# Kernel tuning notes

Measured on AMD Instinct MI355X. Metric: run time of the kernel, lower is better.

Reference implementation:

```python
import jax, jax.numpy as jnp
import numpy as np

H = 64          # hidden_dim
TF = 24         # forecast_length


def _a_norm(N):
    # Complete graph (all i!=j) + GCNConv default self-loops => A+I = ones(N,N).
    # deg_i = N, so D^-1/2 (A+I) D^-1/2 = ones / N. Built generically below.
    A = jnp.ones((N, N), dtype=jnp.float32)
    deg = A.sum(axis=1)
    return A / jnp.sqrt(deg[:, None] * deg[None, :])


def _gcn(x, A, W, b):
    # PyG GCNConv: aggregate(norm * (x W)) + bias
    return jnp.einsum('ij,...jh->...ih', A, x @ W) + b


def setup_inputs() -> dict:
    key = jax.random.key(0)
    ks = jax.random.split(key, 20)
    B, N, T = 32, 128, 96
    s = lambda k, shape, fan: (jax.random.normal(k, shape, jnp.float32) / np.sqrt(max(fan, 1)))
    return {
        'x': jax.random.normal(ks[0], (B, N, T), jnp.float32),
        # spatial GCN stack
        'W_s1': s(ks[1], (1, H), 1), 'b_s1': jnp.zeros((H,), jnp.float32),
        'W_s2': s(ks[2], (H, H), H), 'b_s2': jnp.zeros((H,), jnp.float32),
        # temporal attention MLP
        'Wa1': s(ks[3], (H, H), H), 'ba1': jnp.zeros((H,), jnp.float32),
        'Wa2': s(ks[4], (H, 1), H), 'ba2': jnp.zeros((1,), jnp.float32),
        # GRU (single step, h0 = 0)
        'W_ih': s(ks[5], (3 * H, H), H), 'W_hh': s(ks[6], (3 * H, H), H),
        'b_ih': jnp.zeros((3 * H,), jnp.float32), 'b_hh': jnp.zeros((3 * H,), jnp.float32),
        # ODE-func GCN stack
        'W_o1': s(ks[7], (H, H), H), 'b_o1': jnp.zeros((H,), jnp.float32),
        'W_o2': s(ks[8], (H, H), H), 'b_o2': jnp.zeros((H,), jnp.float32),
        # output head
        'W_out': s(ks[9], (H, 1), H), 'b_out': jnp.zeros((1,), jnp.float32),
    }


def reference(x, W_s1, b_s1, W_s2, b_s2, Wa1, ba1, Wa2, ba2,
              W_ih, W_hh, b_ih, b_hh, W_o1, b_o1, W_o2, b_o2, W_out, b_out):
    B, N, T = x.shape
    A = _a_norm(N)

    # --- spatial encoding, vectorized over (batch, time) ---
    xt = jnp.transpose(x, (0, 2, 1))[..., None]          # (B, T, N, 1)
    h = jax.nn.relu(_gcn(xt, A, W_s1, b_s1))             # (B, T, N, H)
    h = jax.nn.relu(_gcn(h, A, W_s2, b_s2))

    # --- temporal attention over time axis ---
    att = jnp.tanh(h @ Wa1 + ba1) @ Wa2 + ba2            # (B, T, N, 1)
    w = jax.nn.softmax(att, axis=1)
    nf = jnp.sum(h * w, axis=1)                          # (B, N, H)

    # --- one-step GRU encoder with zero initial hidden ---
    gi = nf.reshape(B * N, -1) @ W_ih.T + b_ih           # (B*N, 3H)
    gi_r, gi_z, gi_n = jnp.split(gi, 3, axis=-1)
    bh_r, bh_z, bh_n = jnp.split(b_hh, 3)
    r = jax.nn.sigmoid(gi_r + bh_r)
    z = jax.nn.sigmoid(gi_z + bh_z)
    n = jnp.tanh(gi_n + r * bh_n)
    hidden = ((1.0 - z) * n).reshape(B, N, -1)           # (B, N, H)

    # --- graph ODE derivative: two GCN layers + tanh ---
    def f(y):
        y = jnp.tanh(_gcn(y, A, W_o1, b_o1))
        y = jnp.tanh(_gcn(y, A, W_o2, b_o2))
        return y

    # torchdiffeq fixed-grid 'rk4' (3/8 rule) on t = linspace(0, TF, TF)
    dt = jnp.float32(TF / (TF - 1))
    third = jnp.float32(1.0 / 3.0)

    def step(y, _):
        k1 = f(y)
        k2 = f(y + dt * k1 * third)
        k3 = f(y + dt * (k2 - k1 * third))
        k4 = f(y + dt * (k1 - k2 + k3))
        y1 = y + dt * (k1 + 3.0 * (k2 + k3) + k4) * jnp.float32(0.125)
        return y1, y1

    _, ys = jax.lax.scan(step, hidden, None, length=TF - 1)
    traj = jnp.concatenate([hidden[None], ys], axis=0)   # (TF, B, N, H)

    # output head then rearrange to (B, N, TF)
    preds = (traj @ W_out + b_out)[..., 0]               # (TF, B, N)
    return jnp.transpose(preds, (1, 2, 0))
```

## Files before the change

kernel.cpp:

```cpp
#include <hip/hip_runtime.h>


#define BN 32
#define NN 128
#define TT 96
#define HH 64
#define TFC 24

#if defined(__has_builtin)
#if __has_builtin(__builtin_amdgcn_fdot2)
#define HAVE_FDOT2 1
#endif
#if __has_builtin(__builtin_amdgcn_update_dpp)
#define HAVE_DPP 1
#endif
#endif

using half2v = __fp16 __attribute__((ext_vector_type(2)));
typedef _Float16 half8 __attribute__((ext_vector_type(8)));
typedef float f32x4 __attribute__((ext_vector_type(4)));

__device__ __forceinline__ unsigned pack_pair(float a, float b) {
    union { half2v h; unsigned u; } c;
    c.h = __builtin_amdgcn_cvt_pkrtz(a, b);
    return c.u;
}
__device__ __forceinline__ half2v as_h2(unsigned u) {
    union { unsigned u; half2v h; } c; c.u = u; return c.h;
}
__device__ __forceinline__ unsigned rdlu(unsigned v, int l) {
    return (unsigned)__builtin_amdgcn_readlane((int)v, l);
}
__device__ __forceinline__ float rdl(float v, int l) {
    return __int_as_float(__builtin_amdgcn_readlane(__float_as_int(v), l));
}

template <int CTRL>
__device__ __forceinline__ float dppf(float x) {
#if HAVE_DPP
    return __int_as_float(
        __builtin_amdgcn_update_dpp(0, __float_as_int(x), CTRL, 0xF, 0xF, true));
#else
    return 0.f;
#endif
}

__device__ __forceinline__ float xor1(float x) {
#if HAVE_DPP
    return dppf<0xB1>(x);
#else
    return __shfl_xor(x, 1, 64);
#endif
}

__device__ __forceinline__ float wave_sum(float v) {
#if HAVE_DPP
    v += dppf<0xB1>(v);
    v += dppf<0x4E>(v);
    v += dppf<0x141>(v);
    v += dppf<0x140>(v);
    return ((rdl(v, 0) + rdl(v, 16)) + (rdl(v, 32) + rdl(v, 48)));
#else
#pragma unroll
    for (int off = 32; off > 0; off >>= 1) v += __shfl_xor(v, off, 64);
    return v;
#endif
}
__device__ __forceinline__ void wave_sum2(float& a, float& b) {
#if HAVE_DPP
    a += dppf<0xB1>(a);  b += dppf<0xB1>(b);
    a += dppf<0x4E>(a);  b += dppf<0x4E>(b);
    a += dppf<0x141>(a); b += dppf<0x141>(b);
    a += dppf<0x140>(a); b += dppf<0x140>(b);
    a = (rdl(a, 0) + rdl(a, 16)) + (rdl(a, 32) + rdl(a, 48));
    b = (rdl(b, 0) + rdl(b, 16)) + (rdl(b, 32) + rdl(b, 48));
#else
    a = wave_sum(a); b = wave_sum(b);
#endif
}
__device__ __forceinline__ float wave_max(float v) {
#if HAVE_DPP
    v = fmaxf(v, dppf<0xB1>(v));
    v = fmaxf(v, dppf<0x4E>(v));
    v = fmaxf(v, dppf<0x141>(v));
    v = fmaxf(v, dppf<0x140>(v));
    return fmaxf(fmaxf(rdl(v, 0), rdl(v, 16)), fmaxf(rdl(v, 32), rdl(v, 48)));
#else
#pragma unroll
    for (int off = 32; off > 0; off >>= 1) v = fmaxf(v, __shfl_xor(v, off, 64));
    return v;
#endif
}

__device__ __forceinline__ float dot2acc(unsigned w, unsigned up, float acc) {
#if HAVE_FDOT2
    return __builtin_amdgcn_fdot2(as_h2(w), as_h2(up), acc, false);
#else
    const half2v wh = as_h2(w), uh = as_h2(up);
    return fmaf((float)wh.y, (float)uh.y, fmaf((float)wh.x, (float)uh.x, acc));
#endif
}

#define PMV64_2(WP, UA, UB, RA, RB)                                        \
    do {                                                                   \
        float a0 = 0.f, a1 = 0.f, a2 = 0.f, a3 = 0.f;                      \
        float b0 = 0.f, b1 = 0.f, b2 = 0.f, b3 = 0.f;                      \
        _Pragma("unroll")                                                  \
        for (int k = 0; k < 32; k += 4) {                                  \
            const unsigned ua0 = rdlu(UA, 2 * k);                          \
            const unsigned ub0 = rdlu(UB, 2 * k);                          \
            const unsigned ua1 = rdlu(UA, 2 * k + 2);                      \
            const unsigned ub1 = rdlu(UB, 2 * k + 2);                      \
            const unsigned ua2 = rdlu(UA, 2 * k + 4);                      \
            const unsigned ub2 = rdlu(UB, 2 * k + 4);                      \
            const unsigned ua3 = rdlu(UA, 2 * k + 6);                      \
            const unsigned ub3 = rdlu(UB, 2 * k + 6);                      \
            a0 = dot2acc(WP[k],     ua0, a0);                              \
            b0 = dot2acc(WP[k],     ub0, b0);                              \
            a1 = dot2acc(WP[k + 1], ua1, a1);                              \
            b1 = dot2acc(WP[k + 1], ub1, b1);                              \
            a2 = dot2acc(WP[k + 2], ua2, a2);                              \
            b2 = dot2acc(WP[k + 2], ub2, b2);                              \
            a3 = dot2acc(WP[k + 3], ua3, a3);                              \
            b3 = dot2acc(WP[k + 3], ub3, b3);                              \
        }                                                                  \
        RA = (a0 + a1) + (a2 + a3);                                        \
        RB = (b0 + b1) + (b2 + b3);                                        \
    } while (0)

__device__ __forceinline__ float fast_tanh(float x) {
    float e = __expf(2.f * x);
    return 1.f - 2.f * __builtin_amdgcn_rcpf(e + 1.f);
}
__device__ __forceinline__ float fast_sigmoid(float x) {
    return __builtin_amdgcn_rcpf(1.f + __expf(-x));
}

__global__ __launch_bounds__(256) void spatial_kernel(
    const float* __restrict__ x,    const float* __restrict__ Ws1,
    const float* __restrict__ bs1,  const float* __restrict__ Ws2,
    const float* __restrict__ bs2,  const float* __restrict__ Wa1,
    const float* __restrict__ ba1,  const float* __restrict__ Wa2,
    unsigned* __restrict__ ws_h2,   float* __restrict__ ws_att)
{
    const int tid  = threadIdx.x;
    const int lane = tid & 63;
    const int w    = tid >> 6;
    const int tq   = blockIdx.x;
    const int b    = blockIdx.y;
    const int tbase = tq * 24;

    __shared__ float xbar[24];
    if (tid < 24) {
        const float* xb = x + (size_t)b * NN * TT + (tbase + tid);
        float s = 0.f;
#pragma unroll
        for (int n = 0; n < NN; ++n) s += xb[n * TT];
        xbar[tid] = s * (1.f / 128.f);
    }

    const float ws1l = Ws1[lane];
    const float bs1l = bs1[lane];
    const float bs2l = bs2[lane];
    const float ba1l = ba1[lane];
    const float wa2l = Wa2[lane];
    unsigned ws2p[32], wa1p[32];
#pragma unroll
    for (int k = 0; k < 32; ++k) {
        ws2p[k] = pack_pair(Ws2[(2 * k) * HH + lane], Ws2[(2 * k + 1) * HH + lane]);
        wa1p[k] = pack_pair(Wa1[(2 * k) * HH + lane], Wa1[(2 * k + 1) * HH + lane]);
    }
#pragma unroll
    for (int k = 0; k < 32; ++k) {
        asm volatile("" : "+v"(ws2p[k]), "+v"(wa1p[k]));
    }
    __syncthreads();

#pragma unroll 1
    for (int i = 0; i < 3; ++i) {
        const int tl0 = w * 6 + 2 * i;
        const float sA = xbar[tl0];
        const float sB = xbar[tl0 + 1];
        const float h1A = fmaxf(fmaf(sA, ws1l, bs1l), 0.f);
        const float h1B = fmaxf(fmaf(sB, ws1l, bs1l), 0.f);
        const unsigned uA = pack_pair(h1A, xor1(h1A));
        const unsigned uB = pack_pair(h1B, xor1(h1B));
        float accA, accB;
        PMV64_2(ws2p, uA, uB, accA, accB);
        const float h2A = fmaxf(accA + bs2l, 0.f);
        const float h2B = fmaxf(accB + bs2l, 0.f);
        ws_h2[((size_t)b * (TT / 2) + (tbase + tl0) / 2) * HH + lane] =
            pack_pair(h2A, h2B);

        const unsigned vA = pack_pair(h2A, xor1(h2A));
        const unsigned vB = pack_pair(h2B, xor1(h2B));
        PMV64_2(wa1p, vA, vB, accA, accB);
        float gA = fast_tanh(accA + ba1l) * wa2l;
        float gB = fast_tanh(accB + ba1l) * wa2l;
        wave_sum2(gA, gB);
        if (lane == 0) {
            ws_att[b * TT + tbase + tl0]     = gA;
            ws_att[b * TT + tbase + tl0 + 1] = gB;
        }
    }
}

__global__ __launch_bounds__(64)
__attribute__((amdgpu_waves_per_eu(1, 1)))
void ode_kernel(
    const unsigned* __restrict__ ws_h2, const float* __restrict__ ws_att,
    const float* __restrict__ Wih,  const float* __restrict__ bih,
    const float* __restrict__ bhh,  const float* __restrict__ Wo1,
    const float* __restrict__ bo1p, const float* __restrict__ Wo2,
    const float* __restrict__ bo2p, const float* __restrict__ Wout,
    const float* __restrict__ boutp, float* __restrict__ out)
{
    const int lane = threadIdx.x;
    const int b    = blockIdx.x;

    const float a0s = ws_att[b * TT + lane];
    const float a1s = (lane < TT - 64) ? ws_att[b * TT + 64 + lane] : -1e30f;
    const float m = wave_max(fmaxf(a0s, a1s));
    const float e0 = __expf(a0s - m);
    const float e1 = (lane < TT - 64) ? __expf(a1s - m) : 0.f;
    const float inv = __builtin_amdgcn_rcpf(wave_sum(e0 + e1));
    const float q0 = e0 * inv;
    const float q1 = e1 * inv;

    const unsigned* h2b = ws_h2 + (size_t)b * (TT / 2) * HH;
    unsigned hp[TT / 2];
#pragma unroll
    for (int tp = 0; tp < TT / 2; ++tp) hp[tp] = h2b[tp * HH + lane];
    float nf = 0.f;
#pragma unroll
    for (int tp = 0; tp < 32; ++tp) {
        const unsigned qp = pack_pair(rdl(q0, 2 * tp), rdl(q0, 2 * tp + 1));
        nf = dot2acc(hp[tp], qp, nf);
    }
#pragma unroll
    for (int tp = 32; tp < TT / 2; ++tp) {
        const unsigned qp = pack_pair(rdl(q1, 2 * tp - 64), rdl(q1, 2 * tp - 63));
        nf = dot2acc(hp[tp], qp, nf);
    }

    float gr = bih[lane];
    float gz = bih[64 + lane];
    float gn = bih[128 + lane];
#pragma unroll
    for (int j = 0; j < HH; j += 4) {
        const float4 wr = *(const float4*)&Wih[(size_t)lane * HH + j];
        const float4 wz = *(const float4*)&Wih[(size_t)(64 + lane) * HH + j];
        const float4 wn = *(const float4*)&Wih[(size_t)(128 + lane) * HH + j];
        const float n0 = rdl(nf, j), n1 = rdl(nf, j + 1);
        const float n2 = rdl(nf, j + 2), n3 = rdl(nf, j + 3);
        gr += n0 * wr.x + n1 * wr.y + n2 * wr.z + n3 * wr.w;
        gz += n0 * wz.x + n1 * wz.y + n2 * wz.z + n3 * wz.w;
        gn += n0 * wn.x + n1 * wn.y + n2 * wn.z + n3 * wn.w;
    }
    const float r = fast_sigmoid(gr + bhh[lane]);
    const float z = fast_sigmoid(gz + bhh[64 + lane]);
    const float n = fast_tanh(gn + r * bhh[128 + lane]);
    float y = (1.f - z) * n;

    const int col16 = lane & 15;
    const int grp   = lane >> 4;
    union Frag { unsigned u4[4]; half8 h; };
    Frag B1[4][2], B2[4][2];
#pragma unroll
    for (int t = 0; t < 4; ++t) {
#pragma unroll
        for (int s = 0; s < 2; ++s) {
#pragma unroll
            for (int rr = 0; rr < 4; ++rr) {
                const int k = 32 * s + 8 * grp + 2 * rr;
                const int j = 16 * t + col16;
                B1[t][s].u4[rr] = pack_pair(Wo1[k * HH + j], Wo1[(k + 1) * HH + j]);
                B2[t][s].u4[rr] = pack_pair(Wo2[k * HH + j], Wo2[(k + 1) * HH + j]);
            }
        }
    }
    f32x4 BIAS1[4], BIAS2[4];
#pragma unroll
    for (int t = 0; t < 4; ++t) {
        const float b1v = bo1p[16 * t + col16];
        const float b2v = bo2p[16 * t + col16];
        BIAS1[t] = f32x4{b1v, b1v, b1v, b1v};
        BIAS2[t] = f32x4{b2v, b2v, b2v, b2v};
    }
#pragma unroll
    for (int t = 0; t < 4; ++t) {
#pragma unroll
        for (int s = 0; s < 2; ++s) {
            asm volatile("" : "+v"(B1[t][s].h), "+v"(B2[t][s].h));
        }
        asm volatile("" : "+v"(BIAS1[t]), "+v"(BIAS2[t]));
    }
    const float wo  = Wout[lane];
    const float bo  = boutp[0];

    const int ab0 = 32 * grp;
    const bool s1 = (grp == 1), s2 = (grp == 2), s3 = (grp == 3);
    const f32x4 CZERO = {0.f, 0.f, 0.f, 0.f};

    auto f_eval = [&](float u) -> float {
        Frag A0, A1;
        const unsigned up = pack_pair(u, xor1(u));
#pragma unroll
        for (int rr = 0; rr < 4; ++rr) {
            A0.u4[rr] = (unsigned)__builtin_amdgcn_ds_bpermute(ab0 + 8 * rr, (int)up);
            A1.u4[rr] = (unsigned)__builtin_amdgcn_ds_bpermute(ab0 + 128 + 8 * rr, (int)up);
        }
        f32x4 c0 = __builtin_amdgcn_mfma_f32_16x16x32_f16(A0.h, B1[0][0].h, BIAS1[0], 0, 0, 0);
        f32x4 c1 = __builtin_amdgcn_mfma_f32_16x16x32_f16(A0.h, B1[1][0].h, BIAS1[1], 0, 0, 0);
        f32x4 c2 = __builtin_amdgcn_mfma_f32_16x16x32_f16(A0.h, B1[2][0].h, BIAS1[2], 0, 0, 0);
        f32x4 c3 = __builtin_amdgcn_mfma_f32_16x16x32_f16(A0.h, B1[3][0].h, BIAS1[3], 0, 0, 0);
        f32x4 d0 = __builtin_amdgcn_mfma_f32_16x16x32_f16(A1.h, B1[0][1].h, CZERO, 0, 0, 0);
        f32x4 d1 = __builtin_amdgcn_mfma_f32_16x16x32_f16(A1.h, B1[1][1].h, CZERO, 0, 0, 0);
        f32x4 d2 = __builtin_amdgcn_mfma_f32_16x16x32_f16(A1.h, B1[2][1].h, CZERO, 0, 0, 0);
        f32x4 d3 = __builtin_amdgcn_mfma_f32_16x16x32_f16(A1.h, B1[3][1].h, CZERO, 0, 0, 0);
        const float e0v = c0[0] + d0[0];
        const float e1v = c1[0] + d1[0];
        const float e2v = c2[0] + d2[0];
        const float e3v = c3[0] + d3[0];
        float v = s1 ? e1v : e0v;
        v = s2 ? e2v : v;
        v = s3 ? e3v : v;
        v = fast_tanh(v);
        const unsigned vp = pack_pair(v, xor1(v));
#pragma unroll
        for (int rr = 0; rr < 4; ++rr) {
            A0.u4[rr] = (unsigned)__builtin_amdgcn_ds_bpermute(ab0 + 8 * rr, (int)vp);
            A1.u4[rr] = (unsigned)__builtin_amdgcn_ds_bpermute(ab0 + 128 + 8 * rr, (int)vp);
        }
        c0 = __builtin_amdgcn_mfma_f32_16x16x32_f16(A0.h, B2[0][0].h, BIAS2[0], 0, 0, 0);
        c1 = __builtin_amdgcn_mfma_f32_16x16x32_f16(A0.h, B2[1][0].h, BIAS2[1], 0, 0, 0);
        c2 = __builtin_amdgcn_mfma_f32_16x16x32_f16(A0.h, B2[2][0].h, BIAS2[2], 0, 0, 0);
        c3 = __builtin_amdgcn_mfma_f32_16x16x32_f16(A0.h, B2[3][0].h, BIAS2[3], 0, 0, 0);
        d0 = __builtin_amdgcn_mfma_f32_16x16x32_f16(A1.h, B2[0][1].h, CZERO, 0, 0, 0);
        d1 = __builtin_amdgcn_mfma_f32_16x16x32_f16(A1.h, B2[1][1].h, CZERO, 0, 0, 0);
        d2 = __builtin_amdgcn_mfma_f32_16x16x32_f16(A1.h, B2[2][1].h, CZERO, 0, 0, 0);
        d3 = __builtin_amdgcn_mfma_f32_16x16x32_f16(A1.h, B2[3][1].h, CZERO, 0, 0, 0);
        const float g0v = c0[0] + d0[0];
        const float g1v = c1[0] + d1[0];
        const float g2v = c2[0] + d2[0];
        const float g3v = c3[0] + d3[0];
        float o = s1 ? g1v : g0v;
        o = s2 ? g2v : o;
        o = s3 ? g3v : o;
        return fast_tanh(o);
    };

    float* ob = out + (size_t)b * NN * TFC;
    {
        const float p = wave_sum(y * wo) + bo;
        ob[lane * TFC]        = p;
        ob[(64 + lane) * TFC] = p;
    }

    const float dt = (float)(24.0 / 23.0);
    const float third = 1.f / 3.f;

#pragma unroll 1
    for (int st = 0; st < TFC - 1; ++st) {
        const float k1 = f_eval(y);
        const float k2 = f_eval(y + dt * k1 * third);
        const float k3 = f_eval(y + dt * (k2 - k1 * third));
        const float k4 = f_eval(y + dt * (k1 - k2 + k3));
        y = y + dt * (k1 + 3.f * (k2 + k3) + k4) * 0.125f;
        const float p = wave_sum(y * wo) + bo;
        ob[lane * TFC + st + 1]        = p;
        ob[(64 + lane) * TFC + st + 1] = p;
    }
}

extern "C" void kernel_launch(void* const* d_in, const int* in_sizes, int n_in,
                              void* d_out, int out_size, void* d_ws, size_t ws_size,
                              hipStream_t stream) {
    (void)in_sizes; (void)n_in; (void)ws_size; (void)out_size;
    const float* x    = (const float*)d_in[0];
    const float* Ws1  = (const float*)d_in[1];
    const float* bs1  = (const float*)d_in[2];
    const float* Ws2  = (const float*)d_in[3];
    const float* bs2  = (const float*)d_in[4];
    const float* Wa1  = (const float*)d_in[5];
    const float* ba1  = (const float*)d_in[6];
    const float* Wa2  = (const float*)d_in[7];
    const float* Wih  = (const float*)d_in[9];
    const float* bih  = (const float*)d_in[11];
    const float* bhh  = (const float*)d_in[12];
    const float* Wo1  = (const float*)d_in[13];
    const float* bo1  = (const float*)d_in[14];
    const float* Wo2  = (const float*)d_in[15];
    const float* bo2  = (const float*)d_in[16];
    const float* Wout = (const float*)d_in[17];
    const float* bout = (const float*)d_in[18];

    unsigned* ws_h2 = (unsigned*)d_ws;
    float* ws_att   = (float*)((char*)d_ws + (size_t)BN * (TT / 2) * HH * 4);

    spatial_kernel<<<dim3(4, BN), dim3(256), 0, stream>>>(
        x, Ws1, bs1, Ws2, bs2, Wa1, ba1, Wa2, ws_h2, ws_att);

    ode_kernel<<<dim3(BN), dim3(64), 0, stream>>>(
        ws_h2, ws_att, Wih, bih, bhh, Wo1, bo1, Wo2, bo2, Wout, bout,
        (float*)d_out);
}
```

Measured before the change: 127.5 us.

## Fuse spatial and ODE kernels into one block per batch via LDS

```diff
diff --git a/kernel.cpp b/kernel.cpp
--- a/kernel.cpp
+++ b/kernel.cpp
@@ -13,6 +13,9 @@
 #endif
 #if __has_builtin(__builtin_amdgcn_update_dpp)
 #define HAVE_DPP 1
+#endif
+#if __has_builtin(__builtin_amdgcn_exp2f)
+#define HAVE_EXP2 1
 #endif
 #endif
 
@@ -124,39 +127,84 @@
             a3 = dot2acc(WP[k + 3], ua3, a3);                              \
             b3 = dot2acc(WP[k + 3], ub3, b3);                              \
         }                                                                  \
-        RA = (a0 + a1) + (a2 + a3);                                        \
-        RB = (b0 + b1) + (b2 + b3);                                        \
+        RA = (a0 + a1) + (a2 + a3);                                       \
+        RB = (b0 + b1) + (b2 + b3);                                       \
     } while (0)
 
 __device__ __forceinline__ float fast_tanh(float x) {
+#if HAVE_EXP2
+    float e = __builtin_amdgcn_exp2f(x * 2.885390082f);
+#else
     float e = __expf(2.f * x);
+#endif
     return 1.f - 2.f * __builtin_amdgcn_rcpf(e + 1.f);
 }
 __device__ __forceinline__ float fast_sigmoid(float x) {
     return __builtin_amdgcn_rcpf(1.f + __expf(-x));
 }
 
-__global__ __launch_bounds__(256) void spatial_kernel(
+__global__ __launch_bounds__(512, 1) void fused_kernel(
     const float* __restrict__ x,    const float* __restrict__ Ws1,
     const float* __restrict__ bs1,  const float* __restrict__ Ws2,
     const float* __restrict__ bs2,  const float* __restrict__ Wa1,
     const float* __restrict__ ba1,  const float* __restrict__ Wa2,
-    unsigned* __restrict__ ws_h2,   float* __restrict__ ws_att)
+    const float* __restrict__ Wih,  const float* __restrict__ bih,
+    const float* __restrict__ bhh,  const float* __restrict__ Wo1,
+    const float* __restrict__ bo1p, const float* __restrict__ Wo2,
+    const float* __restrict__ bo2p, const float* __restrict__ Wout,
+    const float* __restrict__ boutp, float* __restrict__ out)
 {
     const int tid  = threadIdx.x;
     const int lane = tid & 63;
     const int w    = tid >> 6;
-    const int tq   = blockIdx.x;
-    const int b    = blockIdx.y;
-    const int tbase = tq * 24;
-
-    __shared__ float xbar[24];
-    if (tid < 24) {
-        const float* xb = x + (size_t)b * NN * TT + (tbase + tid);
+    const int b    = blockIdx.x;
+
+    __shared__ float xbar[TT];
+    __shared__ unsigned h2s[(TT / 2) * HH];
+    __shared__ float atts[TT];
+
+    if (tid < TT) {
+        const float* xb = x + (size_t)b * NN * TT + tid;
         float s = 0.f;
 #pragma unroll
         for (int n = 0; n < NN; ++n) s += xb[n * TT];
         xbar[tid] = s * (1.f / 128.f);
+    }
+
+    const int col16 = lane & 15;
+    const int grp   = lane >> 4;
+    union Frag { unsigned u4[4]; half8 h; };
+    Frag B1[4][2], B2[4][2];
+    f32x4 BIAS1[4], BIAS2[4];
+    if (w == 0) {
+#pragma unroll
+        for (int t = 0; t < 4; ++t) {
+#pragma unroll
+            for (int s = 0; s < 2; ++s) {
+#pragma unroll
+                for (int rr = 0; rr < 4; ++rr) {
+                    const int k = 32 * s + 8 * grp + 2 * rr;
+                    const int j = 16 * t + col16;
+                    B1[t][s].u4[rr] = pack_pair(Wo1[k * HH + j], Wo1[(k + 1) * HH + j]);
+                    B2[t][s].u4[rr] = pack_pair(Wo2[k * HH + j], Wo2[(k + 1) * HH + j]);
+                }
+            }
+        }
+#pragma unroll
+        for (int t = 0; t < 4; ++t) {
+            const float b1v = bo1p[16 * t + col16];
+            const float b2v = bo2p[16 * t + col16];
+            BIAS1[t] = f32x4{b1v, b1v, b1v, b1v};
+            BIAS2[t] = f32x4{b2v, b2v, b2v, b2v};
+        }
+#pragma unroll
+        for (int t = 0; t < 4; ++t) {
+#pragma unroll
+            for (int s = 0; s < 2; ++s) {
+                asm volatile("" : "+v"(B1[t][s].h), "+v"(B2[t][s].h));
+            }
+            asm volatile("" : "+v"(BIAS1[t]), "+v"(BIAS2[t]));
+        }
     }
 
     const float ws1l = Ws1[lane];
@@ -177,8 +225,9 @@
     __syncthreads();
 
 #pragma unroll 1
-    for (int i = 0; i < 3; ++i) {
-        const int tl0 = w * 6 + 2 * i;
+    for (int i = 0; i < 6; ++i) {
+        const int tp  = w * 6 + i;
+        const int tl0 = 2 * tp;
         const float sA = xbar[tl0];
         const float sB = xbar[tl0 + 1];
         const float h1A = fmaxf(fmaf(sA, ws1l, bs1l), 0.f);
@@ -189,8 +238,7 @@
         PMV64_2(ws2p, uA, uB, accA, accB);
         const float h2A = fmaxf(accA + bs2l, 0.f);
         const float h2B = fmaxf(accB + bs2l, 0.f);
-        ws_h2[((size_t)b * (TT / 2) + (tbase + tl0) / 2) * HH + lane] =
-            pack_pair(h2A, h2B);
+        h2s[tp * HH + lane] = pack_pair(h2A, h2B);
 
         const unsigned vA = pack_pair(h2A, xor1(h2A));
         const unsigned vB = pack_pair(h2B, xor1(h2B));
@@ -199,27 +247,16 @@
         float gB = fast_tanh(accB + ba1l) * wa2l;
         wave_sum2(gA, gB);
         if (lane == 0) {
-            ws_att[b * TT + tbase + tl0]     = gA;
-            ws_att[b * TT + tbase + tl0 + 1] = gB;
-        }
-    }
-}
-
-__global__ __launch_bounds__(64)
-__attribute__((amdgpu_waves_per_eu(1, 1)))
-void ode_kernel(
-    const unsigned* __restrict__ ws_h2, const float* __restrict__ ws_att,
-    const float* __restrict__ Wih,  const float* __restrict__ bih,
-    const float* __restrict__ bhh,  const float* __restrict__ Wo1,
-    const float* __restrict__ bo1p, const float* __restrict__ Wo2,
-    const float* __restrict__ bo2p, const float* __restrict__ Wout,
-    const float* __restrict__ boutp, float* __restrict__ out)
-{
-    const int lane = threadIdx.x;
-    const int b    = blockIdx.x;
-
-    const float a0s = ws_att[b * TT + lane];
-    const float a1s = (lane < TT - 64) ? ws_att[b * TT + 64 + lane] : -1e30f;
+            atts[tl0]     = gA;
+            atts[tl0 + 1] = gB;
+        }
+    }
+    __syncthreads();
+
+    if (w != 0) return;
+
+    const float a0s = atts[lane];
+    const float a1s = (lane < TT - 64) ? atts[64 + lane] : -1e30f;
     const float m = wave_max(fmaxf(a0s, a1s));
     const float e0 = __expf(a0s - m);
     const float e1 = (lane < TT - 64) ? __expf(a1s - m) : 0.f;
@@ -227,20 +264,18 @@
     const float q0 = e0 * inv;
     const float q1 = e1 * inv;
 
-    const unsigned* h2b = ws_h2 + (size_t)b * (TT / 2) * HH;
-    unsigned hp[TT / 2];
-#pragma unroll
-    for (int tp = 0; tp < TT / 2; ++tp) hp[tp] = h2b[tp * HH + lane];
     float nf = 0.f;
 #pragma unroll
     for (int tp = 0; tp < 32; ++tp) {
+        const unsigned hpv = h2s[tp * HH + lane];
         const unsigned qp = pack_pair(rdl(q0, 2 * tp), rdl(q0, 2 * tp + 1));
-        nf = dot2acc(hp[tp], qp, nf);
+        nf = dot2acc(hpv, qp, nf);
     }
 #pragma unroll
     for (int tp = 32; tp < TT / 2; ++tp) {
+        const unsigned hpv = h2s[tp * HH + lane];
         const unsigned qp = pack_pair(rdl(q1, 2 * tp - 64), rdl(q1, 2 * tp - 63));
-        nf = dot2acc(hp[tp], qp, nf);
+        nf = dot2acc(hpv, qp, nf);
     }
 
     float gr = bih[lane];
@@ -262,39 +297,6 @@
     const float n = fast_tanh(gn + r * bhh[128 + lane]);
     float y = (1.f - z) * n;
 
-    const int col16 = lane & 15;
-    const int grp   = lane >> 4;
-    union Frag { unsigned u4[4]; half8 h; };
-    Frag B1[4][2], B2[4][2];
-#pragma unroll
-    for (int t = 0; t < 4; ++t) {
-#pragma unroll
-        for (int s = 0; s < 2; ++s) {
-#pragma unroll
-            for (int rr = 0; rr < 4; ++rr) {
-                const int k = 32 * s + 8 * grp + 2 * rr;
-                const int j = 16 * t + col16;
-                B1[t][s].u4[rr] = pack_pair(Wo1[k * HH + j], Wo1[(k + 1) * HH + j]);
-                B2[t][s].u4[rr] = pack_pair(Wo2[k * HH + j], Wo2[(k + 1) * HH + j]);
-            }
-        }
-    }
-    f32x4 BIAS1[4], BIAS2[4];
-#pragma unroll
-    for (int t = 0; t < 4; ++t) {
-        const float b1v = bo1p[16 * t + col16];
-        const float b2v = bo2p[16 * t + col16];
-        BIAS1[t] = f32x4{b1v, b1v, b1v, b1v};
-        BIAS2[t] = f32x4{b2v, b2v, b2v, b2v};
-    }
-#pragma unroll
-    for (int t = 0; t < 4; ++t) {
-#pragma unroll
-        for (int s = 0; s < 2; ++s) {
-            asm volatile("" : "+v"(B1[t][s].h), "+v"(B2[t][s].h));
-        }
-        asm volatile("" : "+v"(BIAS1[t]), "+v"(BIAS2[t]));
-    }
     const float wo  = Wout[lane];
     const float bo  = boutp[0];
 
@@ -376,7 +378,7 @@
 extern "C" void kernel_launch(void* const* d_in, const int* in_sizes, int n_in,
                               void* d_out, int out_size, void* d_ws, size_t ws_size,
                               hipStream_t stream) {
-    (void)in_sizes; (void)n_in; (void)ws_size; (void)out_size;
+    (void)in_sizes; (void)n_in; (void)ws_size; (void)out_size; (void)d_ws;
     const float* x    = (const float*)d_in[0];
     const float* Ws1  = (const float*)d_in[1];
     const float* bs1  = (const float*)d_in[2];
@@ -395,13 +397,8 @@
     const float* Wout = (const float*)d_in[17];
     const float* bout = (const float*)d_in[18];
 
-    unsigned* ws_h2 = (unsigned*)d_ws;
-    float* ws_att   = (float*)((char*)d_ws + (size_t)BN * (TT / 2) * HH * 4);
-
-    spatial_kernel<<<dim3(4, BN), dim3(256), 0, stream>>>(
-        x, Ws1, bs1, Ws2, bs2, Wa1, ba1, Wa2, ws_h2, ws_att);
-
-    ode_kernel<<<dim3(BN), dim3(64), 0, stream>>>(
-        ws_h2, ws_att, Wih, bih, bhh, Wo1, bo1, Wo2, bo2, Wout, bout,
+    fused_kernel<<<dim3(BN), dim3(512), 0, stream>>>(
+        x, Ws1, bs1, Ws2, bs2, Wa1, ba1, Wa2,
+        Wih, bih, bhh, Wo1, bo1, Wo2, bo2, Wout, bout,
         (float*)d_out);
 }
```

Measured after the change: 137.2 us. 1.08x slower.

## Replace ds_bpermute operand shuffles in ODE loop with selector MFMAs and replicated state

Applied to the files above, without the earlier changes.

```diff
diff --git a/kernel.cpp b/kernel.cpp
--- a/kernel.cpp
+++ b/kernel.cpp
@@ -13,6 +13,9 @@
 #endif
 #if __has_builtin(__builtin_amdgcn_update_dpp)
 #define HAVE_DPP 1
+#endif
+#if __has_builtin(__builtin_amdgcn_exp2f)
+#define HAVE_EXP2 1
 #endif
 #endif
 
@@ -124,12 +127,16 @@
             a3 = dot2acc(WP[k + 3], ua3, a3);                              \
             b3 = dot2acc(WP[k + 3], ub3, b3);                              \
         }                                                                  \
-        RA = (a0 + a1) + (a2 + a3);                                        \
-        RB = (b0 + b1) + (b2 + b3);                                        \
+        RA = (a0 + a1) + (a2 + a3);                                       \
+        RB = (b0 + b1) + (b2 + b3);                                       \
     } while (0)
 
 __device__ __forceinline__ float fast_tanh(float x) {
+#if HAVE_EXP2
+    float e = __builtin_amdgcn_exp2f(x * 2.885390082f);
+#else
     float e = __expf(2.f * x);
+#endif
     return 1.f - 2.f * __builtin_amdgcn_rcpf(e + 1.f);
 }
 __device__ __forceinline__ float fast_sigmoid(float x) {
@@ -217,6 +224,8 @@
 {
     const int lane = threadIdx.x;
     const int b    = blockIdx.x;
+    const int col16 = lane & 15;
+    const int grp   = lane >> 4;
 
     const float a0s = ws_att[b * TT + lane];
     const float a1s = (lane < TT - 64) ? ws_att[b * TT + 64 + lane] : -1e30f;
@@ -260,10 +269,13 @@
     const float r = fast_sigmoid(gr + bhh[lane]);
     const float z = fast_sigmoid(gz + bhh[64 + lane]);
     const float n = fast_tanh(gn + r * bhh[128 + lane]);
-    float y = (1.f - z) * n;
-
-    const int col16 = lane & 15;
-    const int grp   = lane >> 4;
+    const float yl = (1.f - z) * n;
+
+    float y0 = __int_as_float(__builtin_amdgcn_ds_bpermute(4 * (col16),      __float_as_int(yl)));
+    float y1 = __int_as_float(__builtin_amdgcn_ds_bpermute(4 * (16 + col16), __float_as_int(yl)));
+    float y2 = __int_as_float(__builtin_amdgcn_ds_bpermute(4 * (32 + col16), __float_as_int(yl)));
+    float y3 = __int_as_float(__builtin_amdgcn_ds_bpermute(4 * (48 + col16), __float_as_int(yl)));
+
     union Frag { unsigned u4[4]; half8 h; };
     Frag B1[4][2], B2[4][2];
 #pragma unroll
@@ -272,12 +284,20 @@
         for (int s = 0; s < 2; ++s) {
 #pragma unroll
             for (int rr = 0; rr < 4; ++rr) {
-                const int k = 32 * s + 8 * grp + 2 * rr;
-                const int j = 16 * t + col16;
-                B1[t][s].u4[rr] = pack_pair(Wo1[k * HH + j], Wo1[(k + 1) * HH + j]);
-                B2[t][s].u4[rr] = pack_pair(Wo2[k * HH + j], Wo2[(k + 1) * HH + j]);
+                const int i0 = 32 * s + 4 * grp + rr;
+                const int i1 = 32 * s + 16 + 4 * grp + rr;
+                const int j  = 16 * t + col16;
+                B1[t][s].u4[rr] = pack_pair(Wo1[i0 * HH + j], Wo1[i1 * HH + j]);
+                B2[t][s].u4[rr] = pack_pair(Wo2[i0 * HH + j], Wo2[i1 * HH + j]);
             }
         }
+    }
+    const unsigned selv = (grp == 0) ? 0x00003C00u : 0u;
+    Frag BS[4];
+#pragma unroll
+    for (int t = 0; t < 4; ++t) {
+#pragma unroll
+        for (int rr = 0; rr < 4; ++rr) BS[t].u4[rr] = (rr == t) ? selv : 0u;
     }
     f32x4 BIAS1[4], BIAS2[4];
 #pragma unroll
@@ -293,81 +313,102 @@
         for (int s = 0; s < 2; ++s) {
             asm volatile("" : "+v"(B1[t][s].h), "+v"(B2[t][s].h));
         }
+        asm volatile("" : "+v"(BS[t].h));
         asm volatile("" : "+v"(BIAS1[t]), "+v"(BIAS2[t]));
     }
-    const float wo  = Wout[lane];
+    const float wo0 = 0.25f * Wout[col16];
+    const float wo1 = 0.25f * Wout[16 + col16];
+    const float wo2 = 0.25f * Wout[32 + col16];
+    const float wo3 = 0.25f * Wout[48 + col16];
     const float bo  = boutp[0];
 
-    const int ab0 = 32 * grp;
-    const bool s1 = (grp == 1), s2 = (grp == 2), s3 = (grp == 3);
     const f32x4 CZERO = {0.f, 0.f, 0.f, 0.f};
 
-    auto f_eval = [&](float u) -> float {
+    auto f_eval = [&](float z0, float z1, float z2, float z3,
+                      float& o0, float& o1, float& o2, float& o3) {
+        Frag Au;
+        Au.u4[0] = pack_pair(z0, z0);
+        Au.u4[1] = pack_pair(z1, z1);
+        Au.u4[2] = pack_pair(z2, z2);
+        Au.u4[3] = pack_pair(z3, z3);
+        f32x4 cb0 = __builtin_amdgcn_mfma_f32_16x16x32_f16(Au.h, BS[0].h, CZERO, 0, 0, 0);
+        f32x4 cb1 = __builtin_amdgcn_mfma_f32_16x16x32_f16(Au.h, BS[1].h, CZERO, 0, 0, 0);
+        f32x4 cb2 = __builtin_amdgcn_mfma_f32_16x16x32_f16(Au.h, BS[2].h, CZERO, 0, 0, 0);
+        f32x4 cb3 = __builtin_amdgcn_mfma_f32_16x16x32_f16(Au.h, BS[3].h, CZERO, 0, 0, 0);
         Frag A0, A1;
-        const unsigned up = pack_pair(u, xor1(u));
 #pragma unroll
         for (int rr = 0; rr < 4; ++rr) {
-            A0.u4[rr] = (unsigned)__builtin_amdgcn_ds_bpermute(ab0 + 8 * rr, (int)up);
-            A1.u4[rr] = (unsigned)__builtin_amdgcn_ds_bpermute(ab0 + 128 + 8 * rr, (int)up);
+            A0.u4[rr] = pack_pair(cb0[rr], cb1[rr]);
+            A1.u4[rr] = pack_pair(cb2[rr], cb3[rr]);
         }
-        f32x4 c0 = __builtin_amdgcn_mfma_f32_16x16x32_f16(A0.h, B1[0][0].h, BIAS1[0], 0, 0, 0);
-        f32x4 c1 = __builtin_amdgcn_mfma_f32_16x16x32_f16(A0.h, B1[1][0].h, BIAS1[1], 0, 0, 0);
-        f32x4 c2 = __builtin_amdgcn_mfma_f32_16x16x32_f16(A0.h, B1[2][0].h, BIAS1[2], 0, 0, 0);
-        f32x4 c3 = __builtin_amdgcn_mfma_f32_16x16x32_f16(A0.h, B1[3][0].h, BIAS1[3], 0, 0, 0);
-        f32x4 d0 = __builtin_amdgcn_mfma_f32_16x16x32_f16(A1.h, B1[0][1].h, CZERO, 0, 0, 0);
-        f32x4 d1 = __builtin_amdgcn_mfma_f32_16x16x32_f16(A1.h, B1[1][1].h, CZERO, 0, 0, 0);
-        f32x4 d2 = __builtin_amdgcn_mfma_f32_16x16x32_f16(A1.h, B1[2][1].h, CZERO, 0, 0, 0);
-        f32x4 d3 = __builtin_amdgcn_mfma_f32_16x16x32_f16(A1.h, B1[3][1].h, CZERO, 0, 0, 0);
-        const float e0v = c0[0] + d0[0];
-        const float e1v = c1[0] + d1[0];
-        const float e2v = c2[0] + d2[0];
-        const float e3v = c3[0] + d3[0];
-        float v = s1 ? e1v : e0v;
-        v = s2 ? e2v : v;
-        v = s3 ? e3v : v;
-        v = fast_tanh(v);
-        const unsigned vp = pack_pair(v, xor1(v));
+        f32x4 c0 = __builtin_amdgcn_mfma_f32_16x16x32_f16(A1.h, B1[0][1].h,
+                   __builtin_amdgcn_mfma_f32_16x16x32_f16(A0.h, B1[0][0].h, BIAS1[0], 0, 0, 0), 0, 0, 0);
+        f32x4 c1 = __builtin_amdgcn_mfma_f32_16x16x32_f16(A1.h, B1[1][1].h,
+                   __builtin_amdgcn_mfma_f32_16x16x32_f16(A0.h, B1[1][0].h, BIAS1[1], 0, 0, 0), 0, 0, 0);
+        f32x4 c2 = __builtin_amdgcn_mfma_f32_16x16x32_f16(A1.h, B1[2][1].h,
+                   __builtin_amdgcn_mfma_f32_16x16x32_f16(A0.h, B1[2][0].h, BIAS1[2], 0, 0, 0), 0, 0, 0);
+        f32x4 c3 = __builtin_amdgcn_mfma_f32_16x16x32_f16(A1.h, B1[3][1].h,
+                   __builtin_amdgcn_mfma_f32_16x16x32_f16(A0.h, B1[3][0].h, BIAS1[3], 0, 0, 0), 0, 0, 0);
+        const float v0 = fast_tanh(c0[0]);
+        const float v1 = fast_tanh(c1[0]);
+        const float v2 = fast_tanh(c2[0]);
+        const float v3 = fast_tanh(c3[0]);
+        Au.u4[0] = pack_pair(v0, v0);
+        Au.u4[1] = pack_pair(v1, v1);
+        Au.u4[2] = pack_pair(v2, v2);
+        Au.u4[3] = pack_pair(v3, v3);
+        cb0 = __builtin_amdgcn_mfma_f32_16x16x32_f16(Au.h, BS[0].h, CZERO, 0, 0, 0);
+        cb1 = __builtin_amdgcn_mfma_f32_16x16x32_f16(Au.h, BS[1].h, CZERO, 0, 0, 0);
+        cb2 = __builtin_amdgcn_mfma_f32_16x16x32_f16(Au.h, BS[2].h, CZERO, 0, 0, 0);
+        cb3 = __builtin_amdgcn_mfma_f32_16x16x32_f16(Au.h, BS[3].h, CZERO, 0, 0, 0);
 #pragma unroll
         for (int rr = 0; rr < 4; ++rr) {
-            A0.u4[rr] = (unsigned)__builtin_amdgcn_ds_bpermute(ab0 + 8 * rr, (int)vp);
-            A1.u4[rr] = (unsigned)__builtin_amdgcn_ds_bpermute(ab0 + 128 + 8 * rr, (int)vp);
+            A0.u4[rr] = pack_pair(cb0[rr], cb1[rr]);
+            A1.u4[rr] = pack_pair(cb2[rr], cb3[rr]);
         }
-        c0 = __builtin_amdgcn_mfma_f32_16x16x32_f16(A0.h, B2[0][0].h, BIAS2[0], 0, 0, 0);
-        c1 = __builtin_amdgcn_mfma_f32_16x16x32_f16(A0.h, B2[1][0].h, BIAS2[1], 0, 0, 0);
-        c2 = __builtin_amdgcn_mfma_f32_16x16x32_f16(A0.h, B2[2][0].h, BIAS2[2], 0, 0, 0);
-        c3 = __builtin_amdgcn_mfma_f32_16x16x32_f16(A0.h, B2[3][0].h, BIAS2[3], 0, 0, 0);
-        d0 = __builtin_amdgcn_mfma_f32_16x16x32_f16(A1.h, B2[0][1].h, CZERO, 0, 0, 0);
-        d1 = __builtin_amdgcn_mfma_f32_16x16x32_f16(A1.h, B2[1][1].h, CZERO, 0, 0, 0);
-        d2 = __builtin_amdgcn_mfma_f32_16x16x32_f16(A1.h, B2[2][1].h, CZERO, 0, 0, 0);
-        d3 = __builtin_amdgcn_mfma_f32_16x16x32_f16(A1.h, B2[3][1].h, CZERO, 0, 0, 0);
-        const float g0v = c0[0] + d0[0];
-        const float g1v = c1[0] + d1[0];
-        const float g2v = c2[0] + d2[0];
-        const float g3v = c3[0] + d3[0];
-        float o = s1 ? g1v : g0v;
-        o = s2 ? g2v : o;
-        o = s3 ? g3v : o;
-        return fast_tanh(o);
+        c0 = __builtin_amdgcn_mfma_f32_16x16x32_f16(A1.h, B2[0][1].h,
+             __builtin_amdgcn_mfma_f32_16x16x32_f16(A0.h, B2[0][0].h, BIAS2[0], 0, 0, 0), 0, 0, 0);
+        c1 = __builtin_amdgcn_mfma_f32_16x16x32_f16(A1.h, B2[1][1].h,
+             __builtin_amdgcn_mfma_f32_16x16x32_f16(A0.h, B2[1][0].h, BIAS2[1], 0, 0, 0), 0, 0, 0);
+        c2 = __builtin_amdgcn_mfma_f32_16x16x32_f16(A1.h, B2[2][1].h,
+             __builtin_amdgcn_mfma_f32_16x16x32_f16(A0.h, B2[2][0].h, BIAS2[2], 0, 0, 0), 0, 0, 0);
+        c3 = __builtin_amdgcn_mfma_f32_16x16x32_f16(A1.h, B2[3][1].h,
+             __builtin_amdgcn_mfma_f32_16x16x32_f16(A0.h, B2[3][0].h, BIAS2[3], 0, 0, 0), 0, 0, 0);
+        o0 = fast_tanh(c0[0]);
+        o1 = fast_tanh(c1[0]);
+        o2 = fast_tanh(c2[0]);
+        o3 = fast_tanh(c3[0]);
     };
 
     float* ob = out + (size_t)b * NN * TFC;
     {
-        const float p = wave_sum(y * wo) + bo;
+        const float p = wave_sum(y0 * wo0 + y1 * wo1 + y2 * wo2 + y3 * wo3) + bo;
         ob[lane * TFC]        = p;
         ob[(64 + lane) * TFC] = p;
     }
 
     const float dt = (float)(24.0 / 23.0);
     const float third = 1.f / 3.f;
+    const float dt3 = dt * third;
 
 #pragma unroll 1
     for (int st = 0; st < TFC - 1; ++st) {
-        const float k1 = f_eval(y);
-        const float k2 = f_eval(y + dt * k1 * third);
-        const float k3 = f_eval(y + dt * (k2 - k1 * third));
-        const float k4 = f_eval(y + dt * (k1 - k2 + k3));
-        y = y + dt * (k1 + 3.f * (k2 + k3) + k4) * 0.125f;
-        const float p = wave_sum(y * wo) + bo;
+        float k10, k11, k12, k13, k20, k21, k22, k23;
+        float k30, k31, k32, k33, k40, k41, k42, k43;
+        f_eval(y0, y1, y2, y3, k10, k11, k12, k13);
+        f_eval(y0 + dt3 * k10, y1 + dt3 * k11, y2 + dt3 * k12, y3 + dt3 * k13,
+               k20, k21, k22, k23);
+        f_eval(y0 + dt * (k20 - third * k10), y1 + dt * (k21 - third * k11),
+               y2 + dt * (k22 - third * k12), y3 + dt * (k23 - third * k13),
+               k30, k31, k32, k33);
+        f_eval(y0 + dt * (k10 - k20 + k30), y1 + dt * (k11 - k21 + k31),
+               y2 + dt * (k12 - k22 + k32), y3 + dt * (k13 - k23 + k33),
+               k40, k41, k42, k43);
+        y0 += dt * (k10 + 3.f * (k20 + k30) + k40) * 0.125f;
+        y1 += dt * (k11 + 3.f * (k21 + k31) + k41) * 0.125f;
+        y2 += dt * (k12 + 3.f * (k22 + k32) + k42) * 0.125f;
+        y3 += dt * (k13 + 3.f * (k23 + k33) + k43) * 0.125f;
+        const float p = wave_sum(y0 * wo0 + y1 * wo1 + y2 * wo2 + y3 * wo3) + bo;
         ob[lane * TFC + st + 1]        = p;
         ob[(64 + lane) * TFC + st + 1] = p;
     }
```

After: 136.8 us. +7.2%, slower.
